# Optimization experiments

Hardware: AMD Instinct MI355X
Metric: run time of the kernel (lower is better)

Reference implementation:

```python
import jax, jax.numpy as jnp
import numpy as np

# Module hyperparameters (from init_kwargs)
IOU_T = 0.5
PROB_T = 0.75
COV = 10.0
TOPK = 500       # self.topk
PRE_K = 2048     # fixed-shape cap on post-threshold candidates entering NMS
B, C, H, W = 4, 4, 160, 160


def setup_inputs() -> dict:
    key = jax.random.key(0)
    k1, k2 = jax.random.split(key)
    mask = jax.random.normal(k1, (B, C, H, W), dtype=jnp.float32)
    # scale bias so boxes have ~10px extent (realistic detections)
    bias = jax.random.normal(k2, (B, 4, H, W), dtype=jnp.float32) * 8.0
    return {"mask": mask, "bias": bias}


def _pos_grid(h, w):
    # equivalent of np.dstack(np.mgrid[0:h, 0:w]) -> [h, w, 2] with (y, x)
    yy, xx = jnp.meshgrid(jnp.arange(h), jnp.arange(w), indexing="ij")
    return jnp.stack([yy, xx], axis=-1).astype(jnp.float32)


def _pairwise_iou(b):
    # b: [K, 4] as (y1, x1, y2, x2); torchvision-style IoU (areas unclamped, inter clamped)
    area = (b[:, 2] - b[:, 0]) * (b[:, 3] - b[:, 1])
    lt = jnp.maximum(b[:, None, :2], b[None, :, :2])
    rb = jnp.minimum(b[:, None, 2:], b[None, :, 2:])
    wh = jnp.clip(rb - lt, 0.0)
    inter = wh[..., 0] * wh[..., 1]
    return inter / (area[:, None] + area[None, :] - inter)


def _nms_keep(iou, valid, thresh):
    # boxes are pre-sorted by descending score; greedy suppression
    K = iou.shape[0]
    idx = jnp.arange(K)
    def body(i, keep):
        sup = (iou[i] > thresh) & (idx > i) & keep[i]
        return keep & ~sup
    return jax.lax.fori_loop(0, K, body, valid)


def _per_image(mask_i, bias_i, pos):
    # mask_i: [C, h, w], bias_i: [4, h, w], pos: [h, w, 2]
    p = jax.nn.softmax(mask_i, axis=0)
    prob = jax.lax.stop_gradient(p.max(axis=0))          # prob.detach()
    cls = p.argmax(axis=0)
    frontal = (cls != 0) & (prob > PROB_T)               # [h, w]
    # boxes = pos tiled to (y,x,y,x) + bias.permute(0,2,3,1)
    boxes = jnp.concatenate([pos, pos], axis=-1) + jnp.transpose(bias_i, (1, 2, 0))
    boxes = boxes.reshape(-1, 4)                          # [h*w, 4]
    score = jnp.where(frontal.reshape(-1), prob.reshape(-1), -1.0)
    # fixed-size candidate set, sorted by descending score (invalid -> -1)
    top_s, idx = jax.lax.top_k(score, PRE_K)
    cand = boxes[idx]
    valid = top_s > 0.0                                   # valid scores > PROB_T > 0
    keep = _nms_keep(_pairwise_iou(cand), valid, IOU_T)
    kept_s = jnp.where(keep, top_s, -1.0)
    fin_s, fi = jax.lax.top_k(kept_s, TOPK)               # min(topk, n) via padding
    fboxes = cand[fi]                                     # [TOPK, 4]
    fvalid = fin_s > 0.0
    fprob = jnp.where(fvalid, fin_s, 0.0)
    mu = (fboxes[:, :2] + fboxes[:, 2:]) * 0.5            # [TOPK, 2]
    sigma = fboxes[:, 2:] - fboxes[:, :2]
    sigma = jnp.where(fvalid[:, None], sigma, 1.0)        # safe divisor for padding
    # gaussian2d: z = (pos - mu) / (sigma / cov); heat = max_n exp(-|z|^2/2) * prob
    z = (pos[None] - mu[:, None, None, :]) / (sigma[:, None, None, :] / COV)  # [TOPK,h,w,2]
    g = jnp.exp(-0.5 * (z ** 2).sum(axis=-1)) * fprob[:, None, None]
    heat = g.max(axis=0)                                  # [h, w]; all-padded -> 0, matches n==0 case
    return heat, fboxes, fvalid


def reference(mask, bias):
    pos = _pos_grid(mask.shape[2], mask.shape[3])
    heat, fboxes, fvalid = jax.vmap(lambda m, b: _per_image(m, b, pos))(mask, bias)
    # original returns (heatmaps, mask, boxes); boxes padded to [B, TOPK, 4] with validity mask
    return heat, mask, fboxes, fvalid
```

## Files before the change

### kernel.cpp

```cpp
#include <hip/hip_runtime.h>
#include <math.h>

#define BATCH 4
#define NCH 4
#define H 160
#define W 160
#define NPIX (H * W)
#define NTILE (NPIX / 256)
#define PRE_K 2048
#define TOPK 500
#define PROB_T 0.75f
#define IOU_T 0.5f
#define COV 10.0f

#define SCORE_OFF 0u
#define KEY_OFF   409600u
#define F_OFF     1228800u
#define CSC_OFF   1261632u
#define CBOX_OFF  1294400u
#define SUP_OFF   1425472u
#define NV_OFF    3523648u
#define PAR_OFF   3523712u
#define FLAG_OFF  3563712u
#define BCNT_OFF  3571904u

#define OUT_HEAT_OFF 0
#define OUT_MASK_OFF 102400
#define OUT_BOX_OFF  512000
#define OUT_VAL_OFF  520000

typedef unsigned long long u64;
typedef unsigned int u32;

__device__ __forceinline__ int block_scan_excl(int v, int tid, int* tmp, int* total) {
    tmp[tid] = v;
    __syncthreads();
    for (int off = 1; off < 256; off <<= 1) {
        int y = (tid >= off) ? tmp[tid - off] : 0;
        __syncthreads();
        tmp[tid] += y;
        __syncthreads();
    }
    int incl = tmp[tid];
    *total = tmp[255];
    __syncthreads();
    return incl - v;
}

__global__ void k_score(const float* __restrict__ mask, float* __restrict__ score,
                        float* __restrict__ out_mask, int* __restrict__ blkcnt) {
    int b = blockIdx.y;
    int pix = blockIdx.x * 256 + threadIdx.x;
    const float* mp = mask + (size_t)b * NCH * NPIX + pix;
    float* op = out_mask + (size_t)b * NCH * NPIX + pix;
    float x0 = mp[0], x1 = mp[NPIX], x2 = mp[2 * NPIX], x3 = mp[3 * NPIX];
    op[0] = x0; op[NPIX] = x1; op[2 * NPIX] = x2; op[3 * NPIX] = x3;
    float m = x0; int c = 0;
    if (x1 > m) { m = x1; c = 1; }
    if (x2 > m) { m = x2; c = 2; }
    if (x3 > m) { m = x3; c = 3; }
    float sum = ((expf(x0 - m) + expf(x1 - m)) + expf(x2 - m)) + expf(x3 - m);
    float prob = 1.0f / sum;
    bool frontal = (c != 0) && (prob > PROB_T);
    score[(size_t)b * NPIX + pix] = frontal ? prob : -1.0f;
    __shared__ int wcnt[4];
    u64 bm = __ballot(frontal);
    if ((threadIdx.x & 63) == 0) wcnt[threadIdx.x >> 6] = __popcll(bm);
    __syncthreads();
    if (threadIdx.x == 0)
        blkcnt[b * NTILE + blockIdx.x] = wcnt[0] + wcnt[1] + wcnt[2] + wcnt[3];
}

__global__ void __launch_bounds__(256)
k_compact(const float* __restrict__ score, const float* __restrict__ bias,
          const int* __restrict__ blkcnt, u64* __restrict__ keys,
          int* __restrict__ Fout, float* __restrict__ cand_score,
          float* __restrict__ cand_box) {
    int b = blockIdx.y;
    int bx = blockIdx.x;
    int tid = threadIdx.x;
    const int* bc = blkcnt + b * NTILE;
    int f_base = 0, F = 0;
    #pragma unroll 4
    for (int k = 0; k < NTILE; ++k) {
        int c = bc[k];
        F += c;
        if (k < bx) f_base += c;
    }
    int pix = bx * 256 + tid;
    float s = score[(size_t)b * NPIX + pix];
    bool fr = (s > 0.0f);
    int lane = tid & 63, wv = tid >> 6;
    int v = fr ? 1 : 0;
    int incl = v;
    for (int off = 1; off < 64; off <<= 1) {
        int y = __shfl_up(incl, off);
        if (lane >= off) incl += y;
    }
    __shared__ int wtot[4];
    __shared__ int wpre[4];
    if (lane == 63) wtot[wv] = incl;
    __syncthreads();
    if (tid == 0) {
        int acc = 0;
        for (int k = 0; k < 4; ++k) { wpre[k] = acc; acc += wtot[k]; }
    }
    __syncthreads();
    int f_local = wpre[wv] + (incl - v);
    if (fr) {
        u32 lo = 0x7FFFFFFFu - (u32)pix;
        keys[(size_t)b * NPIX + f_base + f_local] =
            ((u64)__float_as_uint(s) << 32) | (u64)lo;
    }
    if (bx == 0 && tid == 0) Fout[b] = F;
    if (!fr) {
        int nf_base = bx * 256 - f_base;
        int nf_local = tid - f_local;
        int slot = F + nf_base + nf_local;
        if (slot < PRE_K) {
            const float* bb = bias + (size_t)b * 4 * NPIX;
            cand_score[(size_t)b * PRE_K + slot] = -1.0f;
            float y = (float)(pix / W), x = (float)(pix % W);
            float4 box;
            box.x = y + bb[0 * NPIX + pix];
            box.y = x + bb[1 * NPIX + pix];
            box.z = y + bb[2 * NPIX + pix];
            box.w = x + bb[3 * NPIX + pix];
            ((float4*)cand_box)[(size_t)b * PRE_K + slot] = box;
        }
    }
}

#define RK_CH 4096
__global__ void k_rank(const u64* __restrict__ keys, const float* __restrict__ bias,
                       const int* __restrict__ Fout, float* __restrict__ cand_score,
                       float* __restrict__ cand_box) {
    int b = blockIdx.y;
    int F = Fout[b];
    if (blockIdx.x * 256 >= F) return;
    int i = blockIdx.x * 256 + threadIdx.x;
    const u64* kb = keys + (size_t)b * NPIX;
    u64 ki = (i < F) ? kb[i] : 0;
    int rank = 0;
    __shared__ u64 ks[RK_CH];
    for (int base = 0; base < F; base += RK_CH) {
        int lim = min(RK_CH, F - base);
        __syncthreads();
        for (int k = threadIdx.x; k < lim; k += 256) ks[k] = kb[base + k];
        __syncthreads();
        if (i < F) {
            int k = 0;
            for (; k + 8 <= lim; k += 8) {
                rank += (ks[k]     > ki) ? 1 : 0;
                rank += (ks[k + 1] > ki) ? 1 : 0;
                rank += (ks[k + 2] > ki) ? 1 : 0;
                rank += (ks[k + 3] > ki) ? 1 : 0;
                rank += (ks[k + 4] > ki) ? 1 : 0;
                rank += (ks[k + 5] > ki) ? 1 : 0;
                rank += (ks[k + 6] > ki) ? 1 : 0;
                rank += (ks[k + 7] > ki) ? 1 : 0;
            }
            for (; k < lim; ++k) rank += (ks[k] > ki) ? 1 : 0;
        }
    }
    if (i < F && rank < PRE_K) {
        float si = __uint_as_float((u32)(ki >> 32));
        int xi = 0x7FFFFFFF - (int)(u32)(ki & 0xFFFFFFFFu);
        cand_score[(size_t)b * PRE_K + rank] = si;
        const float* bb = bias + (size_t)b * 4 * NPIX;
        float y = (float)(xi / W), x = (float)(xi % W);
        float4 box;
        box.x = y + bb[0 * NPIX + xi];
        box.y = x + bb[1 * NPIX + xi];
        box.z = y + bb[2 * NPIX + xi];
        box.w = x + bb[3 * NPIX + xi];
        ((float4*)cand_box)[(size_t)b * PRE_K + rank] = box;
    }
}

__global__ void __launch_bounds__(512)
k_iou(const float* __restrict__ cand_box, const int* __restrict__ Fout,
      u32* __restrict__ sup, unsigned char* __restrict__ flag) {
    int b = blockIdx.y;
    int F = Fout[b];
    int V = F < PRE_K ? F : PRE_K;
    int r0 = blockIdx.x * 8;
    if (r0 >= V) return;
    __shared__ float ly1[PRE_K], lx1[PRE_K], ly2[PRE_K], lx2[PRE_K], lar[PRE_K];
    for (int k = threadIdx.x; k < PRE_K; k += 512) {
        float4 v = ((const float4*)cand_box)[(size_t)b * PRE_K + k];
        ly1[k] = v.x; lx1[k] = v.y; ly2[k] = v.z; lx2[k] = v.w;
        lar[k] = (v.z - v.x) * (v.w - v.y);
    }
    __syncthreads();
    int lr = threadIdx.x >> 6;
    int w = threadIdx.x & 63;
    int i = r0 + lr;
    float ay1 = ly1[i], ax1 = lx1[i], ay2 = ly2[i], ax2 = lx2[i], aa = lar[i];
    u32 bits = 0;
    int jbase = w * 32;
    #pragma unroll 4
    for (int jj = 0; jj < 32; ++jj) {
        int jo = (jj + w) & 31;
        int j = jbase + jo;
        if (j > i) {
            float lty = fmaxf(ay1, ly1[j]);
            float ltx = fmaxf(ax1, lx1[j]);
            float rby = fminf(ay2, ly2[j]);
            float rbx = fminf(ax2, lx2[j]);
            float wy = fmaxf(rby - lty, 0.0f);
            float wx = fmaxf(rbx - ltx, 0.0f);
            float inter = wy * wx;
            float iou = inter / ((aa + lar[j]) - inter);
            if (iou > IOU_T) bits |= (1u << jo);
        }
    }
    sup[((size_t)b * PRE_K + i) * 64 + w] = bits;
    bool any = __any(bits != 0u);
    if (w == 0) flag[(size_t)b * PRE_K + i] = any ? 1 : 0;
}

__global__ void __launch_bounds__(256)
k_nmsfin(const u32* __restrict__ sup, const unsigned char* __restrict__ flag,
         const int* __restrict__ Fout, const float* __restrict__ cand_score,
         const float* __restrict__ cand_box, float* __restrict__ out_boxes,
         float* __restrict__ out_valid, float* __restrict__ params,
         int* __restrict__ NV) {
    int b = blockIdx.x;
    int tid = threadIdx.x;
    int F = Fout[b];
    int V = F < PRE_K ? F : PRE_K;
    __shared__ int rid_s[PRE_K];
    __shared__ int M_s;
    __shared__ u32 kws[64];
    __shared__ int tmp[256];

    if (tid < 64) {
        int lane = tid;
        const u32* f32 = (const u32*)(flag + (size_t)b * PRE_K);
        u32 fw[8];
        #pragma unroll
        for (int k = 0; k < 8; ++k) fw[k] = f32[lane * 8 + k];
        int r0 = lane * 32;
        int cnt = 0;
        #pragma unroll
        for (int k = 0; k < 8; ++k)
            #pragma unroll
            for (int j = 0; j < 4; ++j) {
                int r = r0 + k * 4 + j;
                if (((fw[k] >> (8 * j)) & 0xFFu) != 0u && r < V) ++cnt;
            }
        int incl = cnt;
        for (int off = 1; off < 64; off <<= 1) {
            int y = __shfl_up(incl, off);
            if (lane >= off) incl += y;
        }
        if (lane == 63) M_s = incl;
        int pos = incl - cnt;
        #pragma unroll
        for (int k = 0; k < 8; ++k)
            #pragma unroll
            for (int j = 0; j < 4; ++j) {
                int r = r0 + k * 4 + j;
                if (((fw[k] >> (8 * j)) & 0xFFu) != 0u && r < V) rid_s[pos++] = r;
            }
    }
    __syncthreads();

    if (tid < 64) {
        int lane = tid;
        int M = M_s;
        int rem = V - lane * 32;
        u32 kw = (rem >= 32) ? 0xFFFFFFFFu : (rem <= 0 ? 0u : ((1u << rem) - 1u));
        const u32* supb = sup + (size_t)b * PRE_K * 64 + lane;
        int C = (M + 7) >> 3;
        int C4 = (C + 3) & ~3;
        int l7 = lane & 7;
        u32 rbuf[4][8];
        int ridv[4];

        #define LOAD_RID(slot, c) ridv[slot] = rid_s[min((c) * 8 + l7, PRE_K - 1)]
        #define ISSUE(slot) do { \
            _Pragma("unroll") \
            for (int k_ = 0; k_ < 8; ++k_) { \
                int i_ = __builtin_amdgcn_readlane(ridv[slot], k_) & (PRE_K - 1); \
                rbuf[slot][k_] = supb[(size_t)i_ * 64]; \
            } \
        } while (0)
        #define PROC(slot, c) do { \
            _Pragma("unroll") \
            for (int k_ = 0; k_ < 8; ++k_) { \
                int m_ = (c) * 8 + k_; \
                if (m_ < M) { \
                    int i_ = __builtin_amdgcn_readlane(ridv[slot], k_) & (PRE_K - 1); \
                    u32 kb_ = (u32)__builtin_amdgcn_readlane((int)kw, i_ >> 5); \
                    if ((kb_ >> (i_ & 31)) & 1u) kw &= ~rbuf[slot][k_]; \
                } \
            } \
        } while (0)

        LOAD_RID(0, 0); LOAD_RID(1, 1); LOAD_RID(2, 2); LOAD_RID(3, 3);
        ISSUE(0); ISSUE(1); ISSUE(2);
        for (int c = 0; c < C4; c += 4) {
            PROC(0, c);     ISSUE(3);            LOAD_RID(0, c + 4);
            PROC(1, c + 1); ISSUE(0);            LOAD_RID(1, c + 5);
            PROC(2, c + 2); ISSUE(1);            LOAD_RID(2, c + 6);
            PROC(3, c + 3); ISSUE(2);            LOAD_RID(3, c + 7);
        }
        #undef LOAD_RID
        #undef ISSUE
        #undef PROC
        kws[lane] = kw;
    }
    __syncthreads();

    int s0 = tid * 8;
    int bits8 = (int)((kws[s0 >> 5] >> (s0 & 31)) & 0xFFu);
    int cnt = __popc(bits8);
    int tot;
    int kpre = block_scan_excl(cnt, tid, tmp, &tot);
    int NK = tot;
    for (int k = 0; k < 8; ++k) {
        int s = s0 + k;
        int kept = (bits8 >> k) & 1;
        int pos = kept ? kpre : (NK + s - kpre);
        if (pos < TOPK) {
            float4 bx = ((const float4*)cand_box)[(size_t)b * PRE_K + s];
            ((float4*)out_boxes)[(size_t)b * TOPK + pos] = bx;
            out_valid[(size_t)b * TOPK + pos] = kept ? 1.0f : 0.0f;
            if (kept) {
                float scv = cand_score[(size_t)b * PRE_K + s];
                float* pp = params + ((size_t)b * TOPK + pos) * 5;
                pp[0] = (bx.x + bx.z) * 0.5f;
                pp[1] = (bx.y + bx.w) * 0.5f;
                pp[2] = (bx.z - bx.x) / COV;
                pp[3] = (bx.w - bx.y) / COV;
                pp[4] = scv;
            }
        }
        kpre += kept;
    }
    if (tid == 0) NV[b] = NK < TOPK ? NK : TOPK;
}

#define TILE 16
#define TPL (W / TILE)
__global__ void k_heat(const float* __restrict__ params, const int* __restrict__ NV,
                       float* __restrict__ heat) {
    int b = blockIdx.y;
    int ty0 = (blockIdx.x / TPL) * TILE;
    int tx0 = (blockIdx.x % TPL) * TILE;
    int tid = threadIdx.x;
    int nv = NV[b];
    __shared__ float lp[TOPK * 5];
    __shared__ int cntS;
    if (tid == 0) cntS = 0;
    __syncthreads();
    for (int t = tid; t < nv; t += 256) {
        const float* pp = params + ((size_t)b * TOPK + t) * 5;
        float muy = pp[0], mux = pp[1], dy = pp[2], dx = pp[3], p = pp[4];
        float cy = fmaxf(fmaxf((float)ty0 - muy, muy - (float)(ty0 + TILE - 1)), 0.0f);
        float cx = fmaxf(fmaxf((float)tx0 - mux, mux - (float)(tx0 + TILE - 1)), 0.0f);
        float zy = cy / fabsf(dy);
        float zx = cx / fabsf(dx);
        float z2 = zy * zy + zx * zx;
        if (!(z2 > 40.0f)) {
            int idx = atomicAdd(&cntS, 1);
            float* q = lp + idx * 5;
            q[0] = muy; q[1] = mux; q[2] = dy; q[3] = dx; q[4] = p;
        }
    }
    __syncthreads();
    int n = cntS;
    float py = (float)(ty0 + (tid >> 4));
    float px = (float)(tx0 + (tid & 15));
    float m = 0.0f;
    for (int t = 0; t < n; ++t) {
        float muy = lp[t * 5 + 0], mux = lp[t * 5 + 1];
        float dy = lp[t * 5 + 2], dx = lp[t * 5 + 3], p = lp[t * 5 + 4];
        float zy = (py - muy) / dy;
        float zx = (px - mux) / dx;
        float g = expf(-0.5f * (zy * zy + zx * zx)) * p;
        m = fmaxf(m, g);
    }
    heat[(size_t)b * NPIX + (ty0 + (tid >> 4)) * W + tx0 + (tid & 15)] = m;
}

extern "C" void kernel_launch(void* const* d_in, const int* in_sizes, int n_in,
                              void* d_out, int out_size, void* d_ws, size_t ws_size,
                              hipStream_t stream) {
    const float* mask = (const float*)d_in[0];
    const float* bias = (const float*)d_in[1];
    float* out = (float*)d_out;
    char* ws = (char*)d_ws;

    float* score      = (float*)(ws + SCORE_OFF);
    u64*   keys       = (u64*)(ws + KEY_OFF);
    int*   Fout       = (int*)(ws + F_OFF);
    float* cand_score = (float*)(ws + CSC_OFF);
    float* cand_box   = (float*)(ws + CBOX_OFF);
    u32*   sup        = (u32*)(ws + SUP_OFF);
    int*   NV         = (int*)(ws + NV_OFF);
    float* params     = (float*)(ws + PAR_OFF);
    unsigned char* flag = (unsigned char*)(ws + FLAG_OFF);
    int*   blkcnt     = (int*)(ws + BCNT_OFF);

    dim3 g100(NTILE, BATCH);
    k_score<<<g100, 256, 0, stream>>>(mask, score, out + OUT_MASK_OFF, blkcnt);
    k_compact<<<g100, 256, 0, stream>>>(score, bias, blkcnt, keys, Fout,
                                        cand_score, cand_box);
    k_rank<<<g100, 256, 0, stream>>>(keys, bias, Fout, cand_score, cand_box);
    k_iou<<<dim3(PRE_K / 8, BATCH), 512, 0, stream>>>(cand_box, Fout, sup, flag);
    k_nmsfin<<<BATCH, 256, 0, stream>>>(sup, flag, Fout, cand_score, cand_box,
                                        out + OUT_BOX_OFF, out + OUT_VAL_OFF, params, NV);
    k_heat<<<dim3(TPL * (H / TILE), BATCH), 256, 0, stream>>>(params, NV, out + OUT_HEAT_OFF);
}
```

Measured before the change: 115.0 us.

## Fuse all pipeline stages into one cooperative kernel with grid syncs

Measured after the change: 330.3 us. 187% more time.

```diff
diff --git a/kernel.cpp b/kernel.cpp
--- a/kernel.cpp
+++ b/kernel.cpp
@@ -1,5 +1,8 @@
 #include <hip/hip_runtime.h>
+#include <hip/hip_cooperative_groups.h>
 #include <math.h>
+
+namespace cg = cooperative_groups;
 
 #define BATCH 4
 #define NCH 4
@@ -12,10 +15,9 @@
 #define PROB_T 0.75f
 #define IOU_T 0.5f
 #define COV 10.0f
-
-#define SCORE_OFF 0u
+#define RK_CH 4096
+
 #define KEY_OFF   409600u
-#define F_OFF     1228800u
 #define CSC_OFF   1261632u
 #define CBOX_OFF  1294400u
 #define SUP_OFF   1425472u
@@ -29,6 +31,9 @@
 #define OUT_BOX_OFF  512000
 #define OUT_VAL_OFF  520000
 
+#define TILE 16
+#define TPL (W / TILE)
+
 typedef unsigned long long u64;
 typedef unsigned int u32;
 
@@ -47,343 +52,338 @@
     return incl - v;
 }
 
-__global__ void k_score(const float* __restrict__ mask, float* __restrict__ score,
-                        float* __restrict__ out_mask, int* __restrict__ blkcnt) {
-    int b = blockIdx.y;
-    int pix = blockIdx.x * 256 + threadIdx.x;
-    const float* mp = mask + (size_t)b * NCH * NPIX + pix;
-    float* op = out_mask + (size_t)b * NCH * NPIX + pix;
-    float x0 = mp[0], x1 = mp[NPIX], x2 = mp[2 * NPIX], x3 = mp[3 * NPIX];
-    op[0] = x0; op[NPIX] = x1; op[2 * NPIX] = x2; op[3 * NPIX] = x3;
-    float m = x0; int c = 0;
-    if (x1 > m) { m = x1; c = 1; }
-    if (x2 > m) { m = x2; c = 2; }
-    if (x3 > m) { m = x3; c = 3; }
-    float sum = ((expf(x0 - m) + expf(x1 - m)) + expf(x2 - m)) + expf(x3 - m);
-    float prob = 1.0f / sum;
-    bool frontal = (c != 0) && (prob > PROB_T);
-    score[(size_t)b * NPIX + pix] = frontal ? prob : -1.0f;
-    __shared__ int wcnt[4];
-    u64 bm = __ballot(frontal);
-    if ((threadIdx.x & 63) == 0) wcnt[threadIdx.x >> 6] = __popcll(bm);
-    __syncthreads();
-    if (threadIdx.x == 0)
-        blkcnt[b * NTILE + blockIdx.x] = wcnt[0] + wcnt[1] + wcnt[2] + wcnt[3];
-}
-
-__global__ void __launch_bounds__(256)
-k_compact(const float* __restrict__ score, const float* __restrict__ bias,
-          const int* __restrict__ blkcnt, u64* __restrict__ keys,
-          int* __restrict__ Fout, float* __restrict__ cand_score,
-          float* __restrict__ cand_box) {
+union ShMem {
+    struct { int wcnt[4]; } p1;
+    struct { int wtot[4]; int wpre[4]; } p2;
+    u64 ks[RK_CH];
+    struct { float y1[PRE_K], x1[PRE_K], y2[PRE_K], x2[PRE_K], ar[PRE_K]; } p4;
+    struct { int rid[PRE_K]; u32 kws[64]; int tmp[256]; int M; } p5;
+    struct { float lp[TOPK * 5]; int cnt; } p6;
+};
+
+__global__ void __launch_bounds__(256, 2)
+fused(const float* __restrict__ mask, const float* __restrict__ bias,
+      float* __restrict__ out, char* __restrict__ ws)
+{
+    u64*   keys       = (u64*)(ws + KEY_OFF);
+    float* cand_score = (float*)(ws + CSC_OFF);
+    float* cand_box   = (float*)(ws + CBOX_OFF);
+    u32*   sup        = (u32*)(ws + SUP_OFF);
+    int*   NV         = (int*)(ws + NV_OFF);
+    float* params     = (float*)(ws + PAR_OFF);
+    unsigned char* flag = (unsigned char*)(ws + FLAG_OFF);
+    int*   blkcnt     = (int*)(ws + BCNT_OFF);
+    float* heat      = out + OUT_HEAT_OFF;
+    float* out_mask  = out + OUT_MASK_OFF;
+    float* out_boxes = out + OUT_BOX_OFF;
+    float* out_valid = out + OUT_VAL_OFF;
+
+    __shared__ ShMem sh;
+    auto gg = cg::this_grid();
+
     int b = blockIdx.y;
     int bx = blockIdx.x;
     int tid = threadIdx.x;
-    const int* bc = blkcnt + b * NTILE;
-    int f_base = 0, F = 0;
-    #pragma unroll 4
-    for (int k = 0; k < NTILE; ++k) {
-        int c = bc[k];
-        F += c;
-        if (k < bx) f_base += c;
-    }
     int pix = bx * 256 + tid;
-    float s = score[(size_t)b * NPIX + pix];
-    bool fr = (s > 0.0f);
-    int lane = tid & 63, wv = tid >> 6;
-    int v = fr ? 1 : 0;
-    int incl = v;
-    for (int off = 1; off < 64; off <<= 1) {
-        int y = __shfl_up(incl, off);
-        if (lane >= off) incl += y;
-    }
-    __shared__ int wtot[4];
-    __shared__ int wpre[4];
-    if (lane == 63) wtot[wv] = incl;
-    __syncthreads();
-    if (tid == 0) {
-        int acc = 0;
-        for (int k = 0; k < 4; ++k) { wpre[k] = acc; acc += wtot[k]; }
-    }
-    __syncthreads();
-    int f_local = wpre[wv] + (incl - v);
-    if (fr) {
-        u32 lo = 0x7FFFFFFFu - (u32)pix;
-        keys[(size_t)b * NPIX + f_base + f_local] =
-            ((u64)__float_as_uint(s) << 32) | (u64)lo;
-    }
-    if (bx == 0 && tid == 0) Fout[b] = F;
-    if (!fr) {
-        int nf_base = bx * 256 - f_base;
-        int nf_local = tid - f_local;
-        int slot = F + nf_base + nf_local;
-        if (slot < PRE_K) {
-            const float* bb = bias + (size_t)b * 4 * NPIX;
-            cand_score[(size_t)b * PRE_K + slot] = -1.0f;
-            float y = (float)(pix / W), x = (float)(pix % W);
-            float4 box;
-            box.x = y + bb[0 * NPIX + pix];
-            box.y = x + bb[1 * NPIX + pix];
-            box.z = y + bb[2 * NPIX + pix];
-            box.w = x + bb[3 * NPIX + pix];
-            ((float4*)cand_box)[(size_t)b * PRE_K + slot] = box;
-        }
-    }
-}
-
-#define RK_CH 4096
-__global__ void k_rank(const u64* __restrict__ keys, const float* __restrict__ bias,
-                       const int* __restrict__ Fout, float* __restrict__ cand_score,
-                       float* __restrict__ cand_box) {
-    int b = blockIdx.y;
-    int F = Fout[b];
-    if (blockIdx.x * 256 >= F) return;
-    int i = blockIdx.x * 256 + threadIdx.x;
-    const u64* kb = keys + (size_t)b * NPIX;
-    u64 ki = (i < F) ? kb[i] : 0;
-    int rank = 0;
-    __shared__ u64 ks[RK_CH];
-    for (int base = 0; base < F; base += RK_CH) {
-        int lim = min(RK_CH, F - base);
-        __syncthreads();
-        for (int k = threadIdx.x; k < lim; k += 256) ks[k] = kb[base + k];
-        __syncthreads();
-        if (i < F) {
-            int k = 0;
-            for (; k + 8 <= lim; k += 8) {
-                rank += (ks[k]     > ki) ? 1 : 0;
-                rank += (ks[k + 1] > ki) ? 1 : 0;
-                rank += (ks[k + 2] > ki) ? 1 : 0;
-                rank += (ks[k + 3] > ki) ? 1 : 0;
-                rank += (ks[k + 4] > ki) ? 1 : 0;
-                rank += (ks[k + 5] > ki) ? 1 : 0;
-                rank += (ks[k + 6] > ki) ? 1 : 0;
-                rank += (ks[k + 7] > ki) ? 1 : 0;
-            }
-            for (; k < lim; ++k) rank += (ks[k] > ki) ? 1 : 0;
-        }
-    }
-    if (i < F && rank < PRE_K) {
-        float si = __uint_as_float((u32)(ki >> 32));
-        int xi = 0x7FFFFFFF - (int)(u32)(ki & 0xFFFFFFFFu);
-        cand_score[(size_t)b * PRE_K + rank] = si;
-        const float* bb = bias + (size_t)b * 4 * NPIX;
-        float y = (float)(xi / W), x = (float)(xi % W);
-        float4 box;
-        box.x = y + bb[0 * NPIX + xi];
-        box.y = x + bb[1 * NPIX + xi];
-        box.z = y + bb[2 * NPIX + xi];
-        box.w = x + bb[3 * NPIX + xi];
-        ((float4*)cand_box)[(size_t)b * PRE_K + rank] = box;
-    }
-}
-
-__global__ void __launch_bounds__(512)
-k_iou(const float* __restrict__ cand_box, const int* __restrict__ Fout,
-      u32* __restrict__ sup, unsigned char* __restrict__ flag) {
-    int b = blockIdx.y;
-    int F = Fout[b];
-    int V = F < PRE_K ? F : PRE_K;
-    int r0 = blockIdx.x * 8;
-    if (r0 >= V) return;
-    __shared__ float ly1[PRE_K], lx1[PRE_K], ly2[PRE_K], lx2[PRE_K], lar[PRE_K];
-    for (int k = threadIdx.x; k < PRE_K; k += 512) {
-        float4 v = ((const float4*)cand_box)[(size_t)b * PRE_K + k];
-        ly1[k] = v.x; lx1[k] = v.y; ly2[k] = v.z; lx2[k] = v.w;
-        lar[k] = (v.z - v.x) * (v.w - v.y);
-    }
-    __syncthreads();
-    int lr = threadIdx.x >> 6;
-    int w = threadIdx.x & 63;
-    int i = r0 + lr;
-    float ay1 = ly1[i], ax1 = lx1[i], ay2 = ly2[i], ax2 = lx2[i], aa = lar[i];
-    u32 bits = 0;
-    int jbase = w * 32;
-    #pragma unroll 4
-    for (int jj = 0; jj < 32; ++jj) {
-        int jo = (jj + w) & 31;
-        int j = jbase + jo;
-        if (j > i) {
-            float lty = fmaxf(ay1, ly1[j]);
-            float ltx = fmaxf(ax1, lx1[j]);
-            float rby = fminf(ay2, ly2[j]);
-            float rbx = fminf(ax2, lx2[j]);
-            float wy = fmaxf(rby - lty, 0.0f);
-            float wx = fmaxf(rbx - ltx, 0.0f);
-            float inter = wy * wx;
-            float iou = inter / ((aa + lar[j]) - inter);
-            if (iou > IOU_T) bits |= (1u << jo);
-        }
-    }
-    sup[((size_t)b * PRE_K + i) * 64 + w] = bits;
-    bool any = __any(bits != 0u);
-    if (w == 0) flag[(size_t)b * PRE_K + i] = any ? 1 : 0;
-}
-
-__global__ void __launch_bounds__(256)
-k_nmsfin(const u32* __restrict__ sup, const unsigned char* __restrict__ flag,
-         const int* __restrict__ Fout, const float* __restrict__ cand_score,
-         const float* __restrict__ cand_box, float* __restrict__ out_boxes,
-         float* __restrict__ out_valid, float* __restrict__ params,
-         int* __restrict__ NV) {
-    int b = blockIdx.x;
-    int tid = threadIdx.x;
-    int F = Fout[b];
-    int V = F < PRE_K ? F : PRE_K;
-    __shared__ int rid_s[PRE_K];
-    __shared__ int M_s;
-    __shared__ u32 kws[64];
-    __shared__ int tmp[256];
-
-    if (tid < 64) {
-        int lane = tid;
-        const u32* f32 = (const u32*)(flag + (size_t)b * PRE_K);
-        u32 fw[8];
-        #pragma unroll
-        for (int k = 0; k < 8; ++k) fw[k] = f32[lane * 8 + k];
-        int r0 = lane * 32;
-        int cnt = 0;
-        #pragma unroll
-        for (int k = 0; k < 8; ++k)
-            #pragma unroll
-            for (int j = 0; j < 4; ++j) {
-                int r = r0 + k * 4 + j;
-                if (((fw[k] >> (8 * j)) & 0xFFu) != 0u && r < V) ++cnt;
-            }
-        int incl = cnt;
+
+    float sc;
+    bool fr;
+    {
+        const float* mp = mask + (size_t)b * NCH * NPIX + pix;
+        float* op = out_mask + (size_t)b * NCH * NPIX + pix;
+        float x0 = mp[0], x1 = mp[NPIX], x2 = mp[2 * NPIX], x3 = mp[3 * NPIX];
+        op[0] = x0; op[NPIX] = x1; op[2 * NPIX] = x2; op[3 * NPIX] = x3;
+        float mx = x0; int c = 0;
+        if (x1 > mx) { mx = x1; c = 1; }
+        if (x2 > mx) { mx = x2; c = 2; }
+        if (x3 > mx) { mx = x3; c = 3; }
+        float sum = ((expf(x0 - mx) + expf(x1 - mx)) + expf(x2 - mx)) + expf(x3 - mx);
+        float prob = 1.0f / sum;
+        fr = (c != 0) && (prob > PROB_T);
+        sc = prob;
+        u64 bm = __ballot(fr);
+        if ((tid & 63) == 0) sh.p1.wcnt[tid >> 6] = __popcll(bm);
+        __syncthreads();
+        if (tid == 0)
+            blkcnt[b * NTILE + bx] = sh.p1.wcnt[0] + sh.p1.wcnt[1] + sh.p1.wcnt[2] + sh.p1.wcnt[3];
+    }
+    gg.sync();
+
+    int F = 0;
+    {
+        const int* bc = blkcnt + b * NTILE;
+        int f_base = 0;
+        #pragma unroll 4
+        for (int k = 0; k < NTILE; ++k) {
+            int c = bc[k];
+            F += c;
+            if (k < bx) f_base += c;
+        }
+        int lane = tid & 63, wv = tid >> 6;
+        int v = fr ? 1 : 0;
+        int incl = v;
         for (int off = 1; off < 64; off <<= 1) {
             int y = __shfl_up(incl, off);
             if (lane >= off) incl += y;
         }
-        if (lane == 63) M_s = incl;
-        int pos = incl - cnt;
-        #pragma unroll
-        for (int k = 0; k < 8; ++k)
+        if (lane == 63) sh.p2.wtot[wv] = incl;
+        __syncthreads();
+        if (tid == 0) {
+            int acc = 0;
+            for (int k = 0; k < 4; ++k) { sh.p2.wpre[k] = acc; acc += sh.p2.wtot[k]; }
+        }
+        __syncthreads();
+        int f_local = sh.p2.wpre[wv] + (incl - v);
+        if (fr) {
+            u32 lo = 0x7FFFFFFFu - (u32)pix;
+            keys[(size_t)b * NPIX + f_base + f_local] =
+                ((u64)__float_as_uint(sc) << 32) | (u64)lo;
+        }
+        if (!fr) {
+            int nf_base = bx * 256 - f_base;
+            int nf_local = tid - f_local;
+            int slot = F + nf_base + nf_local;
+            if (slot < PRE_K) {
+                const float* bb = bias + (size_t)b * 4 * NPIX;
+                cand_score[(size_t)b * PRE_K + slot] = -1.0f;
+                float y = (float)(pix / W), x = (float)(pix % W);
+                float4 box;
+                box.x = y + bb[0 * NPIX + pix];
+                box.y = x + bb[1 * NPIX + pix];
+                box.z = y + bb[2 * NPIX + pix];
+                box.w = x + bb[3 * NPIX + pix];
+                ((float4*)cand_box)[(size_t)b * PRE_K + slot] = box;
+            }
+        }
+    }
+    gg.sync();
+
+    if (bx * 256 < F) {
+        int i = bx * 256 + tid;
+        const u64* kb = keys + (size_t)b * NPIX;
+        u64 ki = (i < F) ? kb[i] : 0;
+        int rank = 0;
+        for (int base = 0; base < F; base += RK_CH) {
+            int lim = min(RK_CH, F - base);
+            __syncthreads();
+            for (int k = tid; k < lim; k += 256) sh.ks[k] = kb[base + k];
+            __syncthreads();
+            if (i < F) {
+                int k = 0;
+                for (; k + 8 <= lim; k += 8) {
+                    rank += (sh.ks[k]     > ki) ? 1 : 0;
+                    rank += (sh.ks[k + 1] > ki) ? 1 : 0;
+                    rank += (sh.ks[k + 2] > ki) ? 1 : 0;
+                    rank += (sh.ks[k + 3] > ki) ? 1 : 0;
+                    rank += (sh.ks[k + 4] > ki) ? 1 : 0;
+                    rank += (sh.ks[k + 5] > ki) ? 1 : 0;
+                    rank += (sh.ks[k + 6] > ki) ? 1 : 0;
+                    rank += (sh.ks[k + 7] > ki) ? 1 : 0;
+                }
+                for (; k < lim; ++k) rank += (sh.ks[k] > ki) ? 1 : 0;
+            }
+        }
+        if (i < F && rank < PRE_K) {
+            float si = __uint_as_float((u32)(ki >> 32));
+            int xi = 0x7FFFFFFF - (int)(u32)(ki & 0xFFFFFFFFu);
+            cand_score[(size_t)b * PRE_K + rank] = si;
+            const float* bb = bias + (size_t)b * 4 * NPIX;
+            float y = (float)(xi / W), x = (float)(xi % W);
+            float4 box;
+            box.x = y + bb[0 * NPIX + xi];
+            box.y = x + bb[1 * NPIX + xi];
+            box.z = y + bb[2 * NPIX + xi];
+            box.w = x + bb[3 * NPIX + xi];
+            ((float4*)cand_box)[(size_t)b * PRE_K + rank] = box;
+        }
+    }
+    gg.sync();
+
+    int V = F < PRE_K ? F : PRE_K;
+    if (bx * 4 < V) {
+        for (int k = tid; k < PRE_K; k += 256) {
+            float4 v = ((const float4*)cand_box)[(size_t)b * PRE_K + k];
+            sh.p4.y1[k] = v.x; sh.p4.x1[k] = v.y;
+            sh.p4.y2[k] = v.z; sh.p4.x2[k] = v.w;
+            sh.p4.ar[k] = (v.z - v.x) * (v.w - v.y);
+        }
+        __syncthreads();
+        int lr = tid >> 6;
+        int w = tid & 63;
+        for (int i = bx * 4 + lr; i < V; i += NTILE * 4) {
+            float ay1 = sh.p4.y1[i], ax1 = sh.p4.x1[i];
+            float ay2 = sh.p4.y2[i], ax2 = sh.p4.x2[i], aa = sh.p4.ar[i];
+            u32 bits = 0;
+            int jbase = w * 32;
+            #pragma unroll 4
+            for (int jj = 0; jj < 32; ++jj) {
+                int jo = (jj + w) & 31;
+                int j = jbase + jo;
+                if (j > i) {
+                    float lty = fmaxf(ay1, sh.p4.y1[j]);
+                    float ltx = fmaxf(ax1, sh.p4.x1[j]);
+                    float rby = fminf(ay2, sh.p4.y2[j]);
+                    float rbx = fminf(ax2, sh.p4.x2[j]);
+                    float wy = fmaxf(rby - lty, 0.0f);
+                    float wx = fmaxf(rbx - ltx, 0.0f);
+                    float inter = wy * wx;
+                    float iou = inter / ((aa + sh.p4.ar[j]) - inter);
+                    if (iou > IOU_T) bits |= (1u << jo);
+                }
+            }
+            bool any = __any(bits != 0u);
+            if (any) sup[((size_t)b * PRE_K + i) * 64 + w] = bits;
+            if (w == 0) flag[(size_t)b * PRE_K + i] = any ? 1 : 0;
+        }
+    }
+    gg.sync();
+
+    if (bx == 0) {
+        if (tid < 64) {
+            int lane = tid;
+            const u32* f32p = (const u32*)(flag + (size_t)b * PRE_K);
+            u32 fw[8];
             #pragma unroll
-            for (int j = 0; j < 4; ++j) {
-                int r = r0 + k * 4 + j;
-                if (((fw[k] >> (8 * j)) & 0xFFu) != 0u && r < V) rid_s[pos++] = r;
-            }
-    }
-    __syncthreads();
-
-    if (tid < 64) {
-        int lane = tid;
-        int M = M_s;
-        int rem = V - lane * 32;
-        u32 kw = (rem >= 32) ? 0xFFFFFFFFu : (rem <= 0 ? 0u : ((1u << rem) - 1u));
-        const u32* supb = sup + (size_t)b * PRE_K * 64 + lane;
-        int C = (M + 7) >> 3;
-        int C4 = (C + 3) & ~3;
-        int l7 = lane & 7;
-        u32 rbuf[4][8];
-        int ridv[4];
-
-        #define LOAD_RID(slot, c) ridv[slot] = rid_s[min((c) * 8 + l7, PRE_K - 1)]
-        #define ISSUE(slot) do { \
-            _Pragma("unroll") \
-            for (int k_ = 0; k_ < 8; ++k_) { \
-                int i_ = __builtin_amdgcn_readlane(ridv[slot], k_) & (PRE_K - 1); \
-                rbuf[slot][k_] = supb[(size_t)i_ * 64]; \
-            } \
-        } while (0)
-        #define PROC(slot, c) do { \
-            _Pragma("unroll") \
-            for (int k_ = 0; k_ < 8; ++k_) { \
-                int m_ = (c) * 8 + k_; \
-                if (m_ < M) { \
+            for (int k = 0; k < 8; ++k) fw[k] = f32p[lane * 8 + k];
+            int r0 = lane * 32;
+            int cnt = 0;
+            #pragma unroll
+            for (int k = 0; k < 8; ++k)
+                #pragma unroll
+                for (int j = 0; j < 4; ++j) {
+                    int r = r0 + k * 4 + j;
+                    if (((fw[k] >> (8 * j)) & 0xFFu) != 0u && r < V) ++cnt;
+                }
+            int incl = cnt;
+            for (int off = 1; off < 64; off <<= 1) {
+                int y = __shfl_up(incl, off);
+                if (lane >= off) incl += y;
+            }
+            if (lane == 63) sh.p5.M = incl;
+            int pos = incl - cnt;
+            #pragma unroll
+            for (int k = 0; k < 8; ++k)
+                #pragma unroll
+                for (int j = 0; j < 4; ++j) {
+                    int r = r0 + k * 4 + j;
+                    if (((fw[k] >> (8 * j)) & 0xFFu) != 0u && r < V) sh.p5.rid[pos++] = r;
+                }
+        }
+        __syncthreads();
+
+        if (tid < 64) {
+            int lane = tid;
+            int M = sh.p5.M;
+            int rem = V - lane * 32;
+            u32 kw = (rem >= 32) ? 0xFFFFFFFFu : (rem <= 0 ? 0u : ((1u << rem) - 1u));
+            const u32* supb = sup + (size_t)b * PRE_K * 64 + lane;
+            int C = (M + 7) >> 3;
+            int C4 = (C + 3) & ~3;
+            int l7 = lane & 7;
+            u32 rbuf[4][8];
+            int ridv[4];
+
+            #define LOAD_RID(slot, c) ridv[slot] = sh.p5.rid[min((c) * 8 + l7, PRE_K - 1)]
+            #define ISSUE(slot) do { \
+                _Pragma("unroll") \
+                for (int k_ = 0; k_ < 8; ++k_) { \
                     int i_ = __builtin_amdgcn_readlane(ridv[slot], k_) & (PRE_K - 1); \
-                    u32 kb_ = (u32)__builtin_amdgcn_readlane((int)kw, i_ >> 5); \
-                    if ((kb_ >> (i_ & 31)) & 1u) kw &= ~rbuf[slot][k_]; \
+                    rbuf[slot][k_] = supb[(size_t)i_ * 64]; \
                 } \
-            } \
-        } while (0)
-
-        LOAD_RID(0, 0); LOAD_RID(1, 1); LOAD_RID(2, 2); LOAD_RID(3, 3);
-        ISSUE(0); ISSUE(1); ISSUE(2);
-        for (int c = 0; c < C4; c += 4) {
-            PROC(0, c);     ISSUE(3);            LOAD_RID(0, c + 4);
-            PROC(1, c + 1); ISSUE(0);            LOAD_RID(1, c + 5);
-            PROC(2, c + 2); ISSUE(1);            LOAD_RID(2, c + 6);
-            PROC(3, c + 3); ISSUE(2);            LOAD_RID(3, c + 7);
-        }
-        #undef LOAD_RID
-        #undef ISSUE
-        #undef PROC
-        kws[lane] = kw;
-    }
-    __syncthreads();
-
-    int s0 = tid * 8;
-    int bits8 = (int)((kws[s0 >> 5] >> (s0 & 31)) & 0xFFu);
-    int cnt = __popc(bits8);
-    int tot;
-    int kpre = block_scan_excl(cnt, tid, tmp, &tot);
-    int NK = tot;
-    for (int k = 0; k < 8; ++k) {
-        int s = s0 + k;
-        int kept = (bits8 >> k) & 1;
-        int pos = kept ? kpre : (NK + s - kpre);
-        if (pos < TOPK) {
-            float4 bx = ((const float4*)cand_box)[(size_t)b * PRE_K + s];
-            ((float4*)out_boxes)[(size_t)b * TOPK + pos] = bx;
-            out_valid[(size_t)b * TOPK + pos] = kept ? 1.0f : 0.0f;
-            if (kept) {
-                float scv = cand_score[(size_t)b * PRE_K + s];
-                float* pp = params + ((size_t)b * TOPK + pos) * 5;
-                pp[0] = (bx.x + bx.z) * 0.5f;
-                pp[1] = (bx.y + bx.w) * 0.5f;
-                pp[2] = (bx.z - bx.x) / COV;
-                pp[3] = (bx.w - bx.y) / COV;
-                pp[4] = scv;
-            }
-        }
-        kpre += kept;
-    }
-    if (tid == 0) NV[b] = NK < TOPK ? NK : TOPK;
-}
-
-#define TILE 16
-#define TPL (W / TILE)
-__global__ void k_heat(const float* __restrict__ params, const int* __restrict__ NV,
-                       float* __restrict__ heat) {
-    int b = blockIdx.y;
-    int ty0 = (blockIdx.x / TPL) * TILE;
-    int tx0 = (blockIdx.x % TPL) * TILE;
-    int tid = threadIdx.x;
-    int nv = NV[b];
-    __shared__ float lp[TOPK * 5];
-    __shared__ int cntS;
-    if (tid == 0) cntS = 0;
-    __syncthreads();
-    for (int t = tid; t < nv; t += 256) {
-        const float* pp = params + ((size_t)b * TOPK + t) * 5;
-        float muy = pp[0], mux = pp[1], dy = pp[2], dx = pp[3], p = pp[4];
-        float cy = fmaxf(fmaxf((float)ty0 - muy, muy - (float)(ty0 + TILE - 1)), 0.0f);
-        float cx = fmaxf(fmaxf((float)tx0 - mux, mux - (float)(tx0 + TILE - 1)), 0.0f);
-        float zy = cy / fabsf(dy);
-        float zx = cx / fabsf(dx);
-        float z2 = zy * zy + zx * zx;
-        if (!(z2 > 40.0f)) {
-            int idx = atomicAdd(&cntS, 1);
-            float* q = lp + idx * 5;
-            q[0] = muy; q[1] = mux; q[2] = dy; q[3] = dx; q[4] = p;
-        }
-    }
-    __syncthreads();
-    int n = cntS;
-    float py = (float)(ty0 + (tid >> 4));
-    float px = (float)(tx0 + (tid & 15));
-    float m = 0.0f;
-    for (int t = 0; t < n; ++t) {
-        float muy = lp[t * 5 + 0], mux = lp[t * 5 + 1];
-        float dy = lp[t * 5 + 2], dx = lp[t * 5 + 3], p = lp[t * 5 + 4];
-        float zy = (py - muy) / dy;
-        float zx = (px - mux) / dx;
-        float g = expf(-0.5f * (zy * zy + zx * zx)) * p;
-        m = fmaxf(m, g);
-    }
-    heat[(size_t)b * NPIX + (ty0 + (tid >> 4)) * W + tx0 + (tid & 15)] = m;
+            } while (0)
+            #define PROC(slot, c) do { \
+                _Pragma("unroll") \
+                for (int k_ = 0; k_ < 8; ++k_) { \
+                    int m_ = (c) * 8 + k_; \
+                    if (m_ < M) { \
+                        int i_ = __builtin_amdgcn_readlane(ridv[slot], k_) & (PRE_K - 1); \
+                        u32 kb_ = (u32)__builtin_amdgcn_readlane((int)kw, i_ >> 5); \
+                        if ((kb_ >> (i_ & 31)) & 1u) kw &= ~rbuf[slot][k_]; \
+                    } \
+                } \
+            } while (0)
+
+            LOAD_RID(0, 0); LOAD_RID(1, 1); LOAD_RID(2, 2); LOAD_RID(3, 3);
+            ISSUE(0); ISSUE(1); ISSUE(2);
+            for (int c = 0; c < C4; c += 4) {
+                PROC(0, c);     ISSUE(3);            LOAD_RID(0, c + 4);
+                PROC(1, c + 1); ISSUE(0);            LOAD_RID(1, c + 5);
+                PROC(2, c + 2); ISSUE(1);            LOAD_RID(2, c + 6);
+                PROC(3, c + 3); ISSUE(2);            LOAD_RID(3, c + 7);
+            }
+            #undef LOAD_RID
+            #undef ISSUE
+            #undef PROC
+            sh.p5.kws[lane] = kw;
+        }
+        __syncthreads();
+
+        int s0 = tid * 8;
+        int bits8 = (int)((sh.p5.kws[s0 >> 5] >> (s0 & 31)) & 0xFFu);
+        int cnt = __popc(bits8);
+        int tot;
+        int kpre = block_scan_excl(cnt, tid, sh.p5.tmp, &tot);
+        int NK = tot;
+        for (int k = 0; k < 8; ++k) {
+            int s = s0 + k;
+            int kept = (bits8 >> k) & 1;
+            int pos = kept ? kpre : (NK + s - kpre);
+            if (pos < TOPK) {
+                float4 bb4 = ((const float4*)cand_box)[(size_t)b * PRE_K + s];
+                ((float4*)out_boxes)[(size_t)b * TOPK + pos] = bb4;
+                out_valid[(size_t)b * TOPK + pos] = kept ? 1.0f : 0.0f;
+                if (kept) {
+                    float scv = cand_score[(size_t)b * PRE_K + s];
+                    float* pp = params + ((size_t)b * TOPK + pos) * 5;
+                    pp[0] = (bb4.x + bb4.z) * 0.5f;
+                    pp[1] = (bb4.y + bb4.w) * 0.5f;
+                    pp[2] = COV / (bb4.z - bb4.x);
+                    pp[3] = COV / (bb4.w - bb4.y);
+                    pp[4] = scv;
+                }
+            }
+            kpre += kept;
+        }
+        if (tid == 0) NV[b] = NK < TOPK ? NK : TOPK;
+    }
+    gg.sync();
+
+    {
+        int ty0 = (bx / TPL) * TILE;
+        int tx0 = (bx % TPL) * TILE;
+        int nv = NV[b];
+        if (tid == 0) sh.p6.cnt = 0;
+        __syncthreads();
+        for (int t = tid; t < nv; t += 256) {
+            const float* pp = params + ((size_t)b * TOPK + t) * 5;
+            float muy = pp[0], mux = pp[1], ivy = pp[2], ivx = pp[3], p = pp[4];
+            float cy = fmaxf(fmaxf((float)ty0 - muy, muy - (float)(ty0 + TILE - 1)), 0.0f);
+            float cx = fmaxf(fmaxf((float)tx0 - mux, mux - (float)(tx0 + TILE - 1)), 0.0f);
+            float zy = cy * fabsf(ivy);
+            float zx = cx * fabsf(ivx);
+            float z2 = zy * zy + zx * zx;
+            if (!(z2 > 40.0f)) {
+                int idx = atomicAdd(&sh.p6.cnt, 1);
+                float* q = sh.p6.lp + idx * 5;
+                q[0] = muy; q[1] = mux; q[2] = ivy; q[3] = ivx; q[4] = p;
+            }
+        }
+        __syncthreads();
+        int n = sh.p6.cnt;
+        float py = (float)(ty0 + (tid >> 4));
+        float px = (float)(tx0 + (tid & 15));
+        float m = 0.0f;
+        for (int t = 0; t < n; ++t) {
+            float muy = sh.p6.lp[t * 5 + 0], mux = sh.p6.lp[t * 5 + 1];
+            float ivy = sh.p6.lp[t * 5 + 2], ivx = sh.p6.lp[t * 5 + 3];
+            float p = sh.p6.lp[t * 5 + 4];
+            float zy = (py - muy) * ivy;
+            float zx = (px - mux) * ivx;
+            float g = expf(-0.5f * (zy * zy + zx * zx)) * p;
+            m = fmaxf(m, g);
+        }
+        heat[(size_t)b * NPIX + (ty0 + (tid >> 4)) * W + tx0 + (tid & 15)] = m;
+    }
 }
 
 extern "C" void kernel_launch(void* const* d_in, const int* in_sizes, int n_in,
@@ -393,25 +393,7 @@
     const float* bias = (const float*)d_in[1];
     float* out = (float*)d_out;
     char* ws = (char*)d_ws;
-
-    float* score      = (float*)(ws + SCORE_OFF);
-    u64*   keys       = (u64*)(ws + KEY_OFF);
-    int*   Fout       = (int*)(ws + F_OFF);
-    float* cand_score = (float*)(ws + CSC_OFF);
-    float* cand_box   = (float*)(ws + CBOX_OFF);
-    u32*   sup        = (u32*)(ws + SUP_OFF);
-    int*   NV         = (int*)(ws + NV_OFF);
-    float* params     = (float*)(ws + PAR_OFF);
-    unsigned char* flag = (unsigned char*)(ws + FLAG_OFF);
-    int*   blkcnt     = (int*)(ws + BCNT_OFF);
-
-    dim3 g100(NTILE, BATCH);
-    k_score<<<g100, 256, 0, stream>>>(mask, score, out + OUT_MASK_OFF, blkcnt);
-    k_compact<<<g100, 256, 0, stream>>>(score, bias, blkcnt, keys, Fout,
-                                        cand_score, cand_box);
-    k_rank<<<g100, 256, 0, stream>>>(keys, bias, Fout, cand_score, cand_box);
-    k_iou<<<dim3(PRE_K / 8, BATCH), 512, 0, stream>>>(cand_box, Fout, sup, flag);
-    k_nmsfin<<<BATCH, 256, 0, stream>>>(sup, flag, Fout, cand_score, cand_box,
-                                        out + OUT_BOX_OFF, out + OUT_VAL_OFF, params, NV);
-    k_heat<<<dim3(TPL * (H / TILE), BATCH), 256, 0, stream>>>(params, NV, out + OUT_HEAT_OFF);
+    void* args[] = {(void*)&mask, (void*)&bias, (void*)&out, (void*)&ws};
+    hipLaunchCooperativeKernel((void*)fused, dim3(NTILE, BATCH), dim3(256),
+                               args, 0, stream);
 }
```
